# Kernel tuning notes

Measured on AMD Instinct MI355X. Metric: run time of the kernel, lower is better.

Reference implementation:

```python
import jax, jax.numpy as jnp
import numpy as np

HEAD_DIM = 128
MROPE_SECTION = (16, 24, 24)  # sums to HEAD_DIM // 2
ROPE_THETA = 1000000.0
NEG_INF = -2.3819763e38


def _mrope_cos_sin(positions, theta, mrope_section, head_dim):
    # positions: [3, B, T] int; returns cos, sin of shape [B, T, head_dim]
    half = head_dim // 2
    inv_freq = 1.0 / (theta ** (jnp.arange(half, dtype=jnp.float32) * 2.0 / head_dim))
    angles = positions.astype(jnp.float32)[..., None] * inv_freq  # [3, B, T, half]
    sec = np.cumsum([0] + list(mrope_section))
    # pick temporal/height/width channel per frequency band
    angles_sel = jnp.concatenate(
        [angles[j, ..., sec[j]:sec[j + 1]] for j in range(3)], axis=-1
    )  # [B, T, half]
    cos = jnp.cos(angles_sel)
    sin = jnp.sin(angles_sel)
    cos = jnp.concatenate([cos, cos], axis=-1)  # [B, T, head_dim]
    sin = jnp.concatenate([sin, sin], axis=-1)
    return cos, sin


def _apply_rope(x, cos, sin):
    # x: [B, T, n, H]; cos/sin: [B, T, H]
    half = x.shape[-1] // 2
    x1, x2 = x[..., :half], x[..., half:]
    rot = jnp.concatenate([-x2, x1], axis=-1)
    return x * cos[:, :, None, :] + rot * sin[:, :, None, :]


def setup_inputs() -> dict:
    key = jax.random.key(0)
    ks = jax.random.split(key, 8)
    B, T, D = 2, 512, 3584
    N, K, H = 28, 4, 128
    S_CACHE = 3584
    S = S_CACHE + T
    x = jax.random.normal(ks[0], (B, T, D), dtype=jnp.float32)
    wq = jax.random.normal(ks[1], (N, D, H), dtype=jnp.float32) * (D ** -0.5)
    wk = jax.random.normal(ks[2], (K, D, H), dtype=jnp.float32) * (D ** -0.5)
    wv = jax.random.normal(ks[3], (K, D, H), dtype=jnp.float32) * (D ** -0.5)
    wo = jax.random.normal(ks[4], (N, H, D), dtype=jnp.float32) * ((N * H) ** -0.5)
    cache_k = jax.random.normal(ks[5], (B, S_CACHE, K, H), dtype=jnp.float32)
    cache_v = jax.random.normal(ks[6], (B, S_CACHE, K, H), dtype=jnp.float32)
    # positions continue after the cache; all 3 mrope channels identical (text)
    pos1d = S_CACHE + jnp.arange(T, dtype=jnp.int32)
    positions = jnp.broadcast_to(pos1d[None, None, :], (3, B, T))
    # mask: full visibility into cache, causal within the new block
    causal = jnp.tril(jnp.ones((T, T), dtype=bool))
    attn_mask = jnp.concatenate(
        [jnp.ones((T, S_CACHE), dtype=bool), causal], axis=-1
    )[None, None].repeat(B, axis=0)  # [B, 1, T, S]
    return {"x": x, "positions": positions, "attn_mask": attn_mask,
            "cache_k": cache_k, "cache_v": cache_v,
            "wq": wq, "wk": wk, "wv": wv, "wo": wo}


def reference(x, positions, attn_mask, cache_k, cache_v, wq, wk, wv, wo):
    N, K, H = wq.shape[0], wk.shape[0], wq.shape[2]
    G = N // K
    q = jnp.einsum('BTD,NDH->BTNH', x, wq)
    k = jnp.einsum('BSD,KDH->BSKH', x, wk)
    v = jnp.einsum('BSD,KDH->BSKH', x, wv)
    cos, sin = _mrope_cos_sin(positions, ROPE_THETA, MROPE_SECTION, H)
    q = _apply_rope(q, cos, sin)
    k = _apply_rope(k, cos, sin)
    q = q * (H ** -0.5)
    k = jnp.concatenate([cache_k, k], axis=1)  # [B, S, K, H]
    v = jnp.concatenate([cache_v, v], axis=1)
    cached_k, cached_v = k, v
    B, T = q.shape[0], q.shape[1]
    qg = q.reshape(B, T, K, G, H)
    # GQA: broadcast each kv head over its G query-head group (same math as repeat_kv)
    logits = jnp.einsum('BTKGH,BSKH->BKGTS', qg, k,
                        preferred_element_type=jnp.float32)
    masked = jnp.where(attn_mask[:, :, None, :, :], logits, NEG_INF)
    probs = jax.nn.softmax(masked, axis=-1).astype(x.dtype)
    encoded = jnp.einsum('BKGTS,BSKH->BTKGH', probs, v).reshape(B, T, N, H)
    out = jnp.einsum('BTNH,NHD->BTD', encoded, wo)
    return out, cached_k, cached_v
```

## Files before the change

### kernel.cpp

```cpp
#include <hip/hip_runtime.h>
#include <cstdint>
#include <cstddef>
#include <cmath>

typedef __bf16 bf16;
typedef __bf16 bf16x8 __attribute__((ext_vector_type(8)));
typedef float f32x4 __attribute__((ext_vector_type(4)));

__device__ __forceinline__ f32x4 mfma_bf16(bf16x8 a, bf16x8 b, f32x4 c) {
  return __builtin_amdgcn_mfma_f32_16x16x32_bf16(a, b, c, 0, 0, 0);
}

union U8 { bf16 h[8]; uint4 u; };
__device__ __forceinline__ uint4 cvt8(float4 a, float4 b) {
  U8 t;
  t.h[0] = (bf16)a.x; t.h[1] = (bf16)a.y; t.h[2] = (bf16)a.z; t.h[3] = (bf16)a.w;
  t.h[4] = (bf16)b.x; t.h[5] = (bf16)b.y; t.h[6] = (bf16)b.z; t.h[7] = (bf16)b.w;
  return t.u;
}

__device__ __forceinline__ bf16x8 ones8() {
  union { uint4 u; bf16x8 h; } t;
  t.u = make_uint4(0x3F803F80u, 0x3F803F80u, 0x3F803F80u, 0x3F803F80u);
  return t.h;
}

__device__ __forceinline__ void gload_lds16(const bf16* g, bf16* l) {
  __builtin_amdgcn_global_load_lds((const __attribute__((address_space(1))) void*)g,
                                   (__attribute__((address_space(3))) void*)l, 16, 0, 0);
}

__global__ __launch_bounds__(256) void prep(const float* __restrict__ ck,
                                            const float* __restrict__ cv,
                                            float* __restrict__ cko,
                                            float* __restrict__ cvo,
                                            bf16* __restrict__ kb_t,
                                            const float* __restrict__ x,
                                            bf16* __restrict__ xb,
                                            const int* __restrict__ pos,
                                            float* __restrict__ cosb,
                                            float* __restrict__ sinb) {
  size_t idx = (size_t)blockIdx.x * 256 + threadIdx.x;
  size_t e = idx * 8;
  size_t b = e / 1835008u, re = e % 1835008u;
  size_t de = b * 2097152u + re;
  float4 k0 = *(const float4*)(ck + e), k1 = *(const float4*)(ck + e + 4);
  float4 v0 = *(const float4*)(cv + e), v1 = *(const float4*)(cv + e + 4);
  *(float4*)(cko + de) = k0; *(float4*)(cko + de + 4) = k1;
  *(float4*)(cvo + de) = v0; *(float4*)(cvo + de + 4) = v1;
  {
    int s = (int)(re >> 9);
    int rem = (int)(re & 511);
    int khh = rem >> 7, h0 = rem & 127;
    size_t dk = ((size_t)(b * 4 + khh) * 128 + (s >> 5)) * 4096 + (size_t)(s & 31) * 128 + h0;
    *(uint4*)(kb_t + dk) = cvt8(k0, k1);
  }
  *(uint4*)(xb + e) = cvt8(*(const float4*)(x + e), *(const float4*)(x + e + 4));
  if (idx < 65536) {
    int m = (int)(idx >> 6), i = (int)(idx & 63);
    int j = (i < 16) ? 0 : ((i < 40) ? 1 : 2);
    float p = (float)pos[j * 1024 + m];
    float invf = (float)exp((double)i * -0.21586735246819178);
    float a = p * invf;
    cosb[m * 64 + i] = cosf(a);
    sinb[m * 64 + i] = sinf(a);
  }
}

__global__ __launch_bounds__(256) void transpose_f2b(const float* __restrict__ src,
                                                     bf16* __restrict__ dst,
                                                     int R, int C) {
  const size_t ms = (size_t)R * C;
  const float* s = src + (size_t)blockIdx.z * ms;
  bf16* d = dst + (size_t)blockIdx.z * ms;
  const int c0 = blockIdx.x * 64, r0 = blockIdx.y * 64;
  __shared__ bf16 tile[64 * 72];
  const int tid = threadIdx.x;
#pragma unroll
  for (int it = 0; it < 2; ++it) {
    int slot = tid + it * 256;
    int r = slot >> 3, c8 = slot & 7;
    const float* p = s + (size_t)(r0 + r) * C + c0 + c8 * 8;
    *(uint4*)(tile + r * 72 + c8 * 8) = cvt8(*(const float4*)p, *(const float4*)(p + 4));
  }
  __syncthreads();
#pragma unroll
  for (int it = 0; it < 2; ++it) {
    int slot = tid + it * 256;
    int c = slot >> 3, r8 = slot & 7;
    U8 tmp;
#pragma unroll
    for (int jj = 0; jj < 8; ++jj) tmp.h[jj] = tile[(r8 * 8 + jj) * 72 + c];
    *(uint4*)(d + (size_t)(c0 + c) * R + r0 + r8 * 8) = tmp.u;
  }
}

__global__ __launch_bounds__(256) void transpose_qkv(const float* __restrict__ wq,
                                                     const float* __restrict__ wk,
                                                     const float* __restrict__ wv,
                                                     bf16* __restrict__ dst) {
  const size_t ms = (size_t)3584 * 128;
  const int z = blockIdx.z;
  const float* s = (z < 28) ? wq + (size_t)z * ms
                 : (z < 32) ? wk + (size_t)(z - 28) * ms
                            : wv + (size_t)(z - 32) * ms;
  bf16* d = dst + (size_t)z * ms;
  const int c0 = blockIdx.x * 64, r0 = blockIdx.y * 64;
  __shared__ bf16 tile[64 * 72];
  const int tid = threadIdx.x;
#pragma unroll
  for (int it = 0; it < 2; ++it) {
    int slot = tid + it * 256;
    int r = slot >> 3, c8 = slot & 7;
    const float* p = s + (size_t)(r0 + r) * 128 + c0 + c8 * 8;
    *(uint4*)(tile + r * 72 + c8 * 8) = cvt8(*(const float4*)p, *(const float4*)(p + 4));
  }
  __syncthreads();
#pragma unroll
  for (int it = 0; it < 2; ++it) {
    int slot = tid + it * 256;
    int c = slot >> 3, r8 = slot & 7;
    U8 tmp;
#pragma unroll
    for (int jj = 0; jj < 8; ++jj) tmp.h[jj] = tile[(r8 * 8 + jj) * 72 + c];
    *(uint4*)(d + (size_t)(c0 + c) * 3584 + r0 + r8 * 8) = tmp.u;
  }
}

__global__ __launch_bounds__(256) void transpose_v(const float* __restrict__ cvo,
                                                   bf16* __restrict__ vt_t) {
  const int b = blockIdx.z >> 2, kh = blockIdx.z & 3;
  const int s0 = blockIdx.x * 64, h0 = blockIdx.y * 64;
  __shared__ bf16 tile[64 * 72];
  const int tid = threadIdx.x;
#pragma unroll
  for (int it = 0; it < 2; ++it) {
    int slot = tid + it * 256;
    int r = slot >> 3, c8 = slot & 7;
    const float* p = cvo + (size_t)((b * 4096 + s0 + r) * 4 + kh) * 128 + h0 + c8 * 8;
    *(uint4*)(tile + r * 72 + c8 * 8) = cvt8(*(const float4*)p, *(const float4*)(p + 4));
  }
  __syncthreads();
#pragma unroll
  for (int it = 0; it < 2; ++it) {
    int slot = tid + it * 256;
    int c = slot >> 3, r8 = slot & 7;
    U8 tmp;
#pragma unroll
    for (int jj = 0; jj < 8; ++jj) tmp.h[jj] = tile[(r8 * 8 + jj) * 72 + c];
    int s = s0 + r8 * 8;
    *(uint4*)(vt_t + ((size_t)((b * 4 + kh) * 128 + (s >> 5))) * 4096 +
              (size_t)(h0 + c) * 32 + (s & 31)) = tmp.u;
  }
}

template <int MODE>
__global__ __launch_bounds__(256) void gemm64(
    const bf16* __restrict__ A, const bf16* __restrict__ Bt,
    bf16* __restrict__ q_ws, float* __restrict__ cko, bf16* __restrict__ kb_t,
    float* __restrict__ cvo, const float* __restrict__ cosb,
    const float* __restrict__ sinb, float* __restrict__ outp) {
  const int cb = blockIdx.x;
  const int m0 = blockIdx.y * 64;
  const int tid = threadIdx.x;
  const int wave = tid >> 6, lane = tid & 63;
  const int c16 = lane & 15, q4 = lane >> 4;
  __shared__ bf16 lA[2][64 * 64];
  __shared__ bf16 lB[2][128 * 64];

  int offA[2], offB[8][2];
#pragma unroll
  for (int kk = 0; kk < 2; ++kk) offA[kk] = (wave * 16 + c16) * 64 + (kk * 4 + q4) * 8;
#pragma unroll
  for (int j = 0; j < 8; ++j) {
    int rB = j * 16 + c16;
#pragma unroll
    for (int kk = 0; kk < 2; ++kk) offB[j][kk] = rB * 64 + (kk * 4 + q4) * 8;
  }

  f32x4 acc[8];
#pragma unroll
  for (int j = 0; j < 8; ++j) acc[j] = (f32x4){0.f, 0.f, 0.f, 0.f};

  const int srow = tid >> 3, sch = (tid & 7) * 8;
#pragma unroll
  for (int it = 0; it < 2; ++it) {
    int cA = tid + it * 256;
    gload_lds16(A + (size_t)(m0 + (cA >> 3)) * 3584 + (cA & 7) * 8, &lA[0][cA * 8]);
  }
#pragma unroll
  for (int it = 0; it < 4; ++it) {
    int cB = tid + it * 256;
    gload_lds16(Bt + (size_t)(cb * 128 + (cB >> 3)) * 3584 + (cB & 7) * 8, &lB[0][cB * 8]);
  }
  __syncthreads();

  for (int k0 = 0; k0 < 3584; k0 += 64) {
    const int cur = (k0 >> 6) & 1;
    if (k0 + 64 < 3584) {
#pragma unroll
      for (int it = 0; it < 2; ++it) {
        int cA = tid + it * 256;
        gload_lds16(A + (size_t)(m0 + (cA >> 3)) * 3584 + k0 + 64 + (cA & 7) * 8,
                    &lA[cur ^ 1][cA * 8]);
      }
#pragma unroll
      for (int it = 0; it < 4; ++it) {
        int cB = tid + it * 256;
        gload_lds16(Bt + (size_t)(cb * 128 + (cB >> 3)) * 3584 + k0 + 64 + (cB & 7) * 8,
                    &lB[cur ^ 1][cB * 8]);
      }
    }
#pragma unroll
    for (int kk = 0; kk < 2; ++kk) {
      bf16x8 av = *(const bf16x8*)(&lA[cur][offA[kk]]);
#pragma unroll
      for (int j = 0; j < 8; ++j) {
        bf16x8 bv = *(const bf16x8*)(&lB[cur][offB[j][kk]]);
        acc[j] = mfma_bf16(av, bv, acc[j]);
      }
    }
    __syncthreads();
  }

  if (MODE == 1) {
    int mb = m0 + wave * 16 + q4 * 4;
#pragma unroll
    for (int r = 0; r < 4; ++r) {
      size_t rowoff = (size_t)(mb + r) * 3584 + cb * 128;
#pragma unroll
      for (int j = 0; j < 8; ++j) outp[rowoff + j * 16 + c16] = acc[j][r];
    }
    return;
  }

  const int head = cb;
  int mb = m0 + wave * 16 + q4 * 4;
#pragma unroll
  for (int r = 0; r < 4; ++r) {
    int m = mb + r;
    int bb = m >> 9, tt = m & 511;
    if (head < 32) {
      const float* cp = cosb + m * 64;
      const float* sp = sinb + m * 64;
#pragma unroll
      for (int j = 0; j < 4; ++j) {
        int h = j * 16 + c16;
        float c = cp[h], s = sp[h];
        float v1 = acc[j][r], v2 = acc[j + 4][r];
        float o1 = v1 * c - v2 * s;
        float o2 = v2 * c + v1 * s;
        if (head < 28) {
          const float QS = 0.08838834764831845f;
          size_t base = ((size_t)m * 28 + head) * 128;
          q_ws[base + h] = (bf16)(o1 * QS);
          q_ws[base + h + 64] = (bf16)(o2 * QS);
        } else {
          int sg = 3584 + tt;
          size_t base = ((size_t)((bb * 4096 + sg) * 4 + (head - 28))) * 128;
          cko[base + h] = o1;
          cko[base + h + 64] = o2;
          size_t bt = ((size_t)(bb * 4 + (head - 28)) * 128 + (sg >> 5)) * 4096 +
                      (size_t)(sg & 31) * 128;
          kb_t[bt + h] = (bf16)o1;
          kb_t[bt + h + 64] = (bf16)o2;
        }
      }
    } else {
      size_t base = ((size_t)((bb * 4096 + 3584 + tt) * 4 + (head - 32))) * 128;
#pragma unroll
      for (int j = 0; j < 8; ++j) cvo[base + j * 16 + c16] = acc[j][r];
    }
  }
}

__global__ __launch_bounds__(512) void attn_kernel(const bf16* __restrict__ q_ws,
                                                   const bf16* __restrict__ kb_t,
                                                   const bf16* __restrict__ vt_t,
                                                   bf16* __restrict__ enc) {
  const int combo = blockIdx.x & 7;
  const int b = combo >> 2, kh = combo & 3;
  const int t0 = (blockIdx.x >> 3) * 16;
  const int tid = threadIdx.x;
  const int wave = tid >> 6, lane = tid & 63;
  const int c16 = lane & 15, q4 = lane >> 4;

  __shared__ bf16 Kc[2][4096];
  __shared__ bf16 Vc[2][4096];
  __shared__ bf16 Ps[8][16 * 40];

  const int kr = tid >> 4, ksl = tid & 15;
  const int ksrc = kr * 128 + ((ksl ^ (kr & 7)) * 8);
  const int vh = tid >> 2, vsl = tid & 3;
  const int vsrc = vh * 32 + ((vsl ^ ((vh >> 1) & 3)) * 8);
  const bf16* kcb = kb_t + (size_t)((b * 4 + kh) * 128) * 4096;
  const bf16* vcb = vt_t + (size_t)((b * 4 + kh) * 128) * 4096;

  int koff[2][4];
#pragma unroll
  for (int kk = 0; kk < 4; ++kk) {
    int ph = ((q4 * 16 + kk * 64) ^ ((c16 & 7) << 4)) >> 1;
    koff[0][kk] = c16 * 128 + ph;
    koff[1][kk] = (c16 + 16) * 128 + ph;
  }
  int voff[8];
#pragma unroll
  for (int jo = 0; jo < 8; ++jo)
    voff[jo] = (jo * 16 + c16) * 32 + ((q4 ^ ((c16 >> 1) & 3)) * 8);

  const int n = kh * 7 + wave;
  bf16x8 aQ[4];
  if (wave < 7) {
    const bf16* qbase = q_ws + ((size_t)((b * 512 + t0 + c16) * 28 + n)) * 128 + q4 * 8;
#pragma unroll
    for (int kk = 0; kk < 4; ++kk) aQ[kk] = *(const bf16x8*)(qbase + kk * 32);
  }

  f32x4 accO[8];
  f32x4 accL = (f32x4){0.f, 0.f, 0.f, 0.f};
#pragma unroll
  for (int j = 0; j < 8; ++j) accO[j] = (f32x4){0.f, 0.f, 0.f, 0.f};
  const bf16x8 vone = ones8();
  bf16* pw = Ps[wave];

  const int nch = (3631 + t0) >> 5;
  gload_lds16(kcb + ksrc, &Kc[0][tid * 8]);
  gload_lds16(vcb + vsrc, &Vc[0][tid * 8]);
  __syncthreads();

  for (int c = 0; c < nch; ++c) {
    const int cur = c & 1;
    if (c + 1 < nch) {
      gload_lds16(kcb + (size_t)(c + 1) * 4096 + ksrc, &Kc[cur ^ 1][tid * 8]);
      gload_lds16(vcb + (size_t)(c + 1) * 4096 + vsrc, &Vc[cur ^ 1][tid * 8]);
    }
    if (wave < 7) {
      const int s0 = c * 32;
      f32x4 accS0 = (f32x4){0.f, 0.f, 0.f, 0.f};
      f32x4 accS1 = (f32x4){0.f, 0.f, 0.f, 0.f};
#pragma unroll
      for (int kk = 0; kk < 4; ++kk) {
        bf16x8 bK0 = *(const bf16x8*)(&Kc[cur][koff[0][kk]]);
        bf16x8 bK1 = *(const bf16x8*)(&Kc[cur][koff[1][kk]]);
        accS0 = mfma_bf16(aQ[kk], bK0, accS0);
        accS1 = mfma_bf16(aQ[kk], bK1, accS1);
      }

      if (s0 + 31 > 3584 + t0) {
#pragma unroll
        for (int r = 0; r < 4; ++r) {
          int lim = 3584 + t0 + q4 * 4 + r - s0;
          float p0 = (c16 <= lim) ? __expf(accS0[r]) : 0.f;
          float p1 = (16 + c16 <= lim) ? __expf(accS1[r]) : 0.f;
          int prow = (q4 * 4 + r) * 40;
          pw[prow + c16] = (bf16)p0;
          pw[prow + 16 + c16] = (bf16)p1;
        }
      } else {
#pragma unroll
        for (int r = 0; r < 4; ++r) {
          int prow = (q4 * 4 + r) * 40;
          pw[prow + c16] = (bf16)__expf(accS0[r]);
          pw[prow + 16 + c16] = (bf16)__expf(accS1[r]);
        }
      }

      bf16x8 aP = *(const bf16x8*)(pw + c16 * 40 + q4 * 8);
      accL = mfma_bf16(aP, vone, accL);
#pragma unroll
      for (int jo = 0; jo < 8; ++jo) {
        bf16x8 bV = *(const bf16x8*)(&Vc[cur][voff[jo]]);
        accO[jo] = mfma_bf16(aP, bV, accO[jo]);
      }
    }
    __syncthreads();
  }

  if (wave < 7) {
#pragma unroll
    for (int r = 0; r < 4; ++r) {
      float inv = 1.0f / accL[r];
      int tg = t0 + q4 * 4 + r;
      size_t base = ((size_t)((b * 512 + tg) * 28 + n)) * 128;
#pragma unroll
      for (int jo = 0; jo < 8; ++jo)
        enc[base + jo * 16 + c16] = (bf16)(accO[jo][r] * inv);
    }
  }
}

extern "C" void kernel_launch(void* const* d_in, const int* in_sizes, int n_in,
                              void* d_out, int out_size, void* d_ws, size_t ws_size,
                              hipStream_t stream) {
  const float* x = (const float*)d_in[0];
  const int* pos = (const int*)d_in[1];
  const float* ck = (const float*)d_in[3];
  const float* cv = (const float*)d_in[4];
  const float* wq = (const float*)d_in[5];
  const float* wk = (const float*)d_in[6];
  const float* wv = (const float*)d_in[7];
  const float* wo = (const float*)d_in[8];

  float* out = (float*)d_out;
  float* cko = out + 3670016;
  float* cvo = cko + 4194304;

  bf16* wqkvT = (bf16*)d_ws;
  bf16* woT = wqkvT;
  bf16* xb = wqkvT + 16515072;
  bf16* q_ws = xb + 3670016;
  bf16* encw = q_ws + 3670016;
  bf16* kb_t = encw + 3670016;
  bf16* vt_t = kb_t + 4194304;
  float* cosb = (float*)(vt_t + 4194304);
  float* sinb = cosb + 65536;
  if (ws_size < 72351744ull) return;

  prep<<<1792, 256, 0, stream>>>(ck, cv, cko, cvo, kb_t, x, xb, pos, cosb, sinb);
  transpose_qkv<<<dim3(2, 56, 36), 256, 0, stream>>>(wq, wk, wv, wqkvT);
  gemm64<0><<<dim3(36, 16), 256, 0, stream>>>(xb, wqkvT, q_ws, cko, kb_t, cvo, cosb, sinb, nullptr);
  transpose_f2b<<<dim3(56, 56, 1), 256, 0, stream>>>(wo, woT, 3584, 3584);
  transpose_v<<<dim3(64, 2, 8), 256, 0, stream>>>(cvo, vt_t);
  attn_kernel<<<256, 512, 0, stream>>>(q_ws, kb_t, vt_t, encw);
  gemm64<1><<<dim3(28, 16), 256, 0, stream>>>(encw, woT, nullptr, nullptr, nullptr, nullptr,
                                              nullptr, nullptr, out);
}
```

Before: 519.7 us.

## Enlarge GEMM M-tile to 128 and triple-buffer attention K/V loads

The GEMM kernels now compute a 128x128 tile per block, with each wave holding two 16-row A fragments, so every B fragment read from LDS is reused twice. This halves the number of blocks: 288 and 224 instead of 576 and 448. The attention kernel moves from double to triple buffering of K/V chunks, issuing loads two chunks ahead and waiting with explicit vmcnt counters in place of a full syncthreads. The goal is to raise GEMM arithmetic intensity and hide attention memory latency. The cost is lower GEMM occupancy and fewer blocks to fill 256 CUs, plus extra LDS in attention.

```diff
diff --git a/kernel.cpp b/kernel.cpp
--- a/kernel.cpp
+++ b/kernel.cpp
@@ -155,22 +155,26 @@
 }
 
 template <int MODE>
-__global__ __launch_bounds__(256) void gemm64(
+__global__ __launch_bounds__(256) void gemm128(
     const bf16* __restrict__ A, const bf16* __restrict__ Bt,
     bf16* __restrict__ q_ws, float* __restrict__ cko, bf16* __restrict__ kb_t,
     float* __restrict__ cvo, const float* __restrict__ cosb,
     const float* __restrict__ sinb, float* __restrict__ outp) {
   const int cb = blockIdx.x;
-  const int m0 = blockIdx.y * 64;
+  const int m0 = blockIdx.y * 128;
   const int tid = threadIdx.x;
   const int wave = tid >> 6, lane = tid & 63;
   const int c16 = lane & 15, q4 = lane >> 4;
-  __shared__ bf16 lA[2][64 * 64];
+  __shared__ bf16 lA[2][128 * 64];
   __shared__ bf16 lB[2][128 * 64];
 
-  int offA[2], offB[8][2];
-#pragma unroll
-  for (int kk = 0; kk < 2; ++kk) offA[kk] = (wave * 16 + c16) * 64 + (kk * 4 + q4) * 8;
+  int offA[2][2], offB[8][2];
+#pragma unroll
+  for (int i = 0; i < 2; ++i) {
+    int rA = wave * 32 + i * 16 + c16;
+#pragma unroll
+    for (int kk = 0; kk < 2; ++kk) offA[i][kk] = rA * 64 + (kk * 4 + q4) * 8;
+  }
 #pragma unroll
   for (int j = 0; j < 8; ++j) {
     int rB = j * 16 + c16;
@@ -178,20 +182,17 @@
     for (int kk = 0; kk < 2; ++kk) offB[j][kk] = rB * 64 + (kk * 4 + q4) * 8;
   }
 
-  f32x4 acc[8];
-#pragma unroll
-  for (int j = 0; j < 8; ++j) acc[j] = (f32x4){0.f, 0.f, 0.f, 0.f};
-
-  const int srow = tid >> 3, sch = (tid & 7) * 8;
-#pragma unroll
-  for (int it = 0; it < 2; ++it) {
-    int cA = tid + it * 256;
-    gload_lds16(A + (size_t)(m0 + (cA >> 3)) * 3584 + (cA & 7) * 8, &lA[0][cA * 8]);
-  }
+  f32x4 acc[2][8];
+#pragma unroll
+  for (int i = 0; i < 2; ++i)
+#pragma unroll
+    for (int j = 0; j < 8; ++j) acc[i][j] = (f32x4){0.f, 0.f, 0.f, 0.f};
+
 #pragma unroll
   for (int it = 0; it < 4; ++it) {
-    int cB = tid + it * 256;
-    gload_lds16(Bt + (size_t)(cb * 128 + (cB >> 3)) * 3584 + (cB & 7) * 8, &lB[0][cB * 8]);
+    int slot = tid + it * 256;
+    gload_lds16(A + (size_t)(m0 + (slot >> 3)) * 3584 + (slot & 7) * 8, &lA[0][slot * 8]);
+    gload_lds16(Bt + (size_t)(cb * 128 + (slot >> 3)) * 3584 + (slot & 7) * 8, &lB[0][slot * 8]);
   }
   __syncthreads();
 
@@ -199,77 +200,81 @@
     const int cur = (k0 >> 6) & 1;
     if (k0 + 64 < 3584) {
 #pragma unroll
-      for (int it = 0; it < 2; ++it) {
-        int cA = tid + it * 256;
-        gload_lds16(A + (size_t)(m0 + (cA >> 3)) * 3584 + k0 + 64 + (cA & 7) * 8,
-                    &lA[cur ^ 1][cA * 8]);
-      }
-#pragma unroll
       for (int it = 0; it < 4; ++it) {
-        int cB = tid + it * 256;
-        gload_lds16(Bt + (size_t)(cb * 128 + (cB >> 3)) * 3584 + k0 + 64 + (cB & 7) * 8,
-                    &lB[cur ^ 1][cB * 8]);
+        int slot = tid + it * 256;
+        gload_lds16(A + (size_t)(m0 + (slot >> 3)) * 3584 + k0 + 64 + (slot & 7) * 8,
+                    &lA[cur ^ 1][slot * 8]);
+        gload_lds16(Bt + (size_t)(cb * 128 + (slot >> 3)) * 3584 + k0 + 64 + (slot & 7) * 8,
+                    &lB[cur ^ 1][slot * 8]);
       }
     }
 #pragma unroll
     for (int kk = 0; kk < 2; ++kk) {
-      bf16x8 av = *(const bf16x8*)(&lA[cur][offA[kk]]);
+      bf16x8 av0 = *(const bf16x8*)(&lA[cur][offA[0][kk]]);
+      bf16x8 av1 = *(const bf16x8*)(&lA[cur][offA[1][kk]]);
 #pragma unroll
       for (int j = 0; j < 8; ++j) {
         bf16x8 bv = *(const bf16x8*)(&lB[cur][offB[j][kk]]);
-        acc[j] = mfma_bf16(av, bv, acc[j]);
+        acc[0][j] = mfma_bf16(av0, bv, acc[0][j]);
+        acc[1][j] = mfma_bf16(av1, bv, acc[1][j]);
       }
     }
     __syncthreads();
   }
 
   if (MODE == 1) {
-    int mb = m0 + wave * 16 + q4 * 4;
+#pragma unroll
+    for (int i = 0; i < 2; ++i) {
+      int mb = m0 + wave * 32 + i * 16 + q4 * 4;
+#pragma unroll
+      for (int r = 0; r < 4; ++r) {
+        size_t rowoff = (size_t)(mb + r) * 3584 + cb * 128;
+#pragma unroll
+        for (int j = 0; j < 8; ++j) outp[rowoff + j * 16 + c16] = acc[i][j][r];
+      }
+    }
+    return;
+  }
+
+  const int head = cb;
+#pragma unroll
+  for (int i = 0; i < 2; ++i) {
+    int mb = m0 + wave * 32 + i * 16 + q4 * 4;
 #pragma unroll
     for (int r = 0; r < 4; ++r) {
-      size_t rowoff = (size_t)(mb + r) * 3584 + cb * 128;
-#pragma unroll
-      for (int j = 0; j < 8; ++j) outp[rowoff + j * 16 + c16] = acc[j][r];
-    }
-    return;
-  }
-
-  const int head = cb;
-  int mb = m0 + wave * 16 + q4 * 4;
-#pragma unroll
-  for (int r = 0; r < 4; ++r) {
-    int m = mb + r;
-    int bb = m >> 9, tt = m & 511;
-    if (head < 32) {
-      const float* cp = cosb + m * 64;
-      const float* sp = sinb + m * 64;
-#pragma unroll
-      for (int j = 0; j < 4; ++j) {
-        int h = j * 16 + c16;
-        float c = cp[h], s = sp[h];
-        float v1 = acc[j][r], v2 = acc[j + 4][r];
-        float o1 = v1 * c - v2 * s;
-        float o2 = v2 * c + v1 * s;
-        if (head < 28) {
-          const float QS = 0.08838834764831845f;
-          size_t base = ((size_t)m * 28 + head) * 128;
-          q_ws[base + h] = (bf16)(o1 * QS);
-          q_ws[base + h + 64] = (bf16)(o2 * QS);
-        } else {
-          int sg = 3584 + tt;
-          size_t base = ((size_t)((bb * 4096 + sg) * 4 + (head - 28))) * 128;
-          cko[base + h] = o1;
-          cko[base + h + 64] = o2;
-          size_t bt = ((size_t)(bb * 4 + (head - 28)) * 128 + (sg >> 5)) * 4096 +
-                      (size_t)(sg & 31) * 128;
-          kb_t[bt + h] = (bf16)o1;
-          kb_t[bt + h + 64] = (bf16)o2;
+      int m = mb + r;
+      int bb = m >> 9, tt = m & 511;
+      if (head < 32) {
+        const float* cp = cosb + m * 64;
+        const float* sp = sinb + m * 64;
+#pragma unroll
+        for (int j = 0; j < 4; ++j) {
+          int h = j * 16 + c16;
+          float c = cp[h], s = sp[h];
+          float v1 = acc[i][j][r], v2 = acc[i][j + 4][r];
+          float o1 = v1 * c - v2 * s;
+          float o2 = v2 * c + v1 * s;
+          if (head < 28) {
+            const float QS = 0.08838834764831845f;
+            size_t base = ((size_t)m * 28 + head) * 128;
+            q_ws[base + h] = (bf16)(o1 * QS);
+            q_ws[base + h + 64] = (bf16)(o2 * QS);
+          } else {
+            int sg = 3584 + tt;
+            size_t base = ((size_t)((bb * 4096 + sg) * 4 + (head - 28))) * 128;
+            cko[base + h] = o1;
+            cko[base + h + 64] = o2;
+            size_t bt = ((size_t)(bb * 4 + (head - 28)) * 128 + (sg >> 5)) * 4096 +
+                        (size_t)(sg & 31) * 128;
+            kb_t[bt + h] = (bf16)o1;
+            kb_t[bt + h + 64] = (bf16)o2;
+          }
         }
-      }
-    } else {
-      size_t base = ((size_t)((bb * 4096 + 3584 + tt) * 4 + (head - 32))) * 128;
-#pragma unroll
-      for (int j = 0; j < 8; ++j) cvo[base + j * 16 + c16] = acc[j][r];
+      } else {
+        size_t base = ((size_t)((bb * 4096 + 3584 + tt) * 4 + (head - 32))) * 128;
+#pragma unroll
+        for (int j = 0; j < 8; ++j) cvo[base + j * 16 + c16] = acc[i][j][r];
+      }
     }
   }
 }
@@ -285,8 +290,8 @@
   const int wave = tid >> 6, lane = tid & 63;
   const int c16 = lane & 15, q4 = lane >> 4;
 
-  __shared__ bf16 Kc[2][4096];
-  __shared__ bf16 Vc[2][4096];
+  __shared__ bf16 Kc[3][4096];
+  __shared__ bf16 Vc[3][4096];
   __shared__ bf16 Ps[8][16 * 40];
 
   const int kr = tid >> 4, ksl = tid & 15;
@@ -324,24 +329,33 @@
   bf16* pw = Ps[wave];
 
   const int nch = (3631 + t0) >> 5;
+
   gload_lds16(kcb + ksrc, &Kc[0][tid * 8]);
   gload_lds16(vcb + vsrc, &Vc[0][tid * 8]);
-  __syncthreads();
-
+  gload_lds16(kcb + 4096 + ksrc, &Kc[1][tid * 8]);
+  gload_lds16(vcb + 4096 + vsrc, &Vc[1][tid * 8]);
+  asm volatile("s_waitcnt vmcnt(2)" ::: "memory");
+  __builtin_amdgcn_sched_barrier(0);
+  __builtin_amdgcn_s_barrier();
+  __builtin_amdgcn_sched_barrier(0);
+
+  int cur = 0, nx2 = 2;
   for (int c = 0; c < nch; ++c) {
-    const int cur = c & 1;
-    if (c + 1 < nch) {
-      gload_lds16(kcb + (size_t)(c + 1) * 4096 + ksrc, &Kc[cur ^ 1][tid * 8]);
-      gload_lds16(vcb + (size_t)(c + 1) * 4096 + vsrc, &Vc[cur ^ 1][tid * 8]);
+    {
+      int cn = (c + 2 < nch) ? c + 2 : nch - 1;
+      gload_lds16(kcb + (size_t)cn * 4096 + ksrc, &Kc[nx2][tid * 8]);
+      gload_lds16(vcb + (size_t)cn * 4096 + vsrc, &Vc[nx2][tid * 8]);
     }
     if (wave < 7) {
       const int s0 = c * 32;
+      const bf16* kc = Kc[cur];
+      const bf16* vc = Vc[cur];
       f32x4 accS0 = (f32x4){0.f, 0.f, 0.f, 0.f};
       f32x4 accS1 = (f32x4){0.f, 0.f, 0.f, 0.f};
 #pragma unroll
       for (int kk = 0; kk < 4; ++kk) {
-        bf16x8 bK0 = *(const bf16x8*)(&Kc[cur][koff[0][kk]]);
-        bf16x8 bK1 = *(const bf16x8*)(&Kc[cur][koff[1][kk]]);
+        bf16x8 bK0 = *(const bf16x8*)(&kc[koff[0][kk]]);
+        bf16x8 bK1 = *(const bf16x8*)(&kc[koff[1][kk]]);
         accS0 = mfma_bf16(aQ[kk], bK0, accS0);
         accS1 = mfma_bf16(aQ[kk], bK1, accS1);
       }
@@ -369,11 +383,17 @@
       accL = mfma_bf16(aP, vone, accL);
 #pragma unroll
       for (int jo = 0; jo < 8; ++jo) {
-        bf16x8 bV = *(const bf16x8*)(&Vc[cur][voff[jo]]);
+        bf16x8 bV = *(const bf16x8*)(&vc[voff[jo]]);
         accO[jo] = mfma_bf16(aP, bV, accO[jo]);
       }
     }
-    __syncthreads();
+    asm volatile("s_waitcnt lgkmcnt(0)" ::: "memory");
+    asm volatile("s_waitcnt vmcnt(2)" ::: "memory");
+    __builtin_amdgcn_sched_barrier(0);
+    __builtin_amdgcn_s_barrier();
+    __builtin_amdgcn_sched_barrier(0);
+    cur = (cur == 2) ? 0 : cur + 1;
+    nx2 = (nx2 == 2) ? 0 : nx2 + 1;
   }
 
   if (wave < 7) {
@@ -418,10 +438,10 @@
 
   prep<<<1792, 256, 0, stream>>>(ck, cv, cko, cvo, kb_t, x, xb, pos, cosb, sinb);
   transpose_qkv<<<dim3(2, 56, 36), 256, 0, stream>>>(wq, wk, wv, wqkvT);
-  gemm64<0><<<dim3(36, 16), 256, 0, stream>>>(xb, wqkvT, q_ws, cko, kb_t, cvo, cosb, sinb, nullptr);
+  gemm128<0><<<dim3(36, 8), 256, 0, stream>>>(xb, wqkvT, q_ws, cko, kb_t, cvo, cosb, sinb, nullptr);
   transpose_f2b<<<dim3(56, 56, 1), 256, 0, stream>>>(wo, woT, 3584, 3584);
   transpose_v<<<dim3(64, 2, 8), 256, 0, stream>>>(cvo, vt_t);
   attn_kernel<<<256, 512, 0, stream>>>(q_ws, kb_t, vt_t, encw);
-  gemm64<1><<<dim3(28, 16), 256, 0, stream>>>(encw, woT, nullptr, nullptr, nullptr, nullptr,
+  gemm128<1><<<dim3(28, 8), 256, 0, stream>>>(encw, woT, nullptr, nullptr, nullptr, nullptr,
                                               nullptr, nullptr, out);
 }
```

Result: faster. 502.4 us (-3.3%).
